# Performance work log

Measured on AMD Instinct MI355X. Metric: run time of the kernel, lower is better.

## Reference

```python
import jax, jax.numpy as jnp
import numpy as np


def setup_inputs() -> dict:
    key = jax.random.key(0)
    k1, k2, k3 = jax.random.split(key, 3)
    B, S, D, H = 16, 2048, 1024, 1024
    inp = jax.random.normal(k1, (B, S, D), dtype=jnp.float32)
    W = jax.random.normal(k2, (3 * H, D), dtype=jnp.float32) * (1.0 / np.sqrt(D))
    b = jax.random.normal(k3, (3 * H,), dtype=jnp.float32) * 0.01
    return {"inp": inp, "W": W, "b": b}


def _forget_mult(z, f):
    # z, f: [B, S, H]; h_t = f_t*z_t + (1-f_t)*h_{t-1}, h_{-1}=0 (hid=None)
    zT = jnp.swapaxes(z, 0, 1)  # [S, B, H]
    fT = jnp.swapaxes(f, 0, 1)

    def step(h, zf):
        z_t, f_t = zf
        h = f_t * z_t + (1.0 - f_t) * h
        return h, h

    h0 = jnp.zeros_like(zT[0])
    _, cT = jax.lax.scan(step, h0, (zT, fT))
    return jnp.swapaxes(cT, 0, 1)  # [B, S, H]


def reference(inp, W, b):
    # window=1, batch_first=True, output_gate=True, backward=False, hid=None
    y = jnp.einsum('bsd,hd->bsh', inp, W) + b  # [B, S, 3H]
    z_gate, f_gate, o_gate = jnp.split(y, 3, axis=2)
    z_gate = jnp.tanh(z_gate)
    f_gate = jax.nn.sigmoid(f_gate)
    c_gate = _forget_mult(z_gate, f_gate)
    output = jax.nn.sigmoid(o_gate) * c_gate
    return output, c_gate[:, -1]
```

## Files before the change

kernel.cpp:

```cpp
#include <hip/hip_runtime.h>


typedef unsigned short ushort_t;
typedef _Float16 half_t;
typedef __bf16 bf16x8 __attribute__((ext_vector_type(8)));
typedef float f32x4 __attribute__((ext_vector_type(4)));
typedef ushort_t us8 __attribute__((ext_vector_type(8)));
typedef half_t f16x4 __attribute__((ext_vector_type(4)));

__device__ __forceinline__ ushort_t f2bf(float f) {
  unsigned int x = __builtin_bit_cast(unsigned int, f);
  x += 0x7fffu + ((x >> 16) & 1u);
  return (ushort_t)(x >> 16);
}
__device__ __forceinline__ float bf2f(ushort_t u) {
  unsigned int x = ((unsigned int)u) << 16;
  return __builtin_bit_cast(float, x);
}
__device__ __forceinline__ void storeg(float* p, float v) { *p = v; }
__device__ __forceinline__ void storeg(half_t* p, float v) { *p = (half_t)v; }

__device__ __forceinline__ f32x4 loadg4(const float* p) {
  return *(const f32x4*)p;
}
__device__ __forceinline__ f32x4 loadg4(const half_t* p) {
  const f16x4 v = *(const f16x4*)p;
  f32x4 r;
  r[0] = (float)v[0]; r[1] = (float)v[1]; r[2] = (float)v[2]; r[3] = (float)v[3];
  return r;
}
__device__ __forceinline__ f32x4 fma4(f32x4 a, f32x4 b, f32x4 c) {
  f32x4 r;
#pragma unroll
  for (int k = 0; k < 4; ++k) r[k] = fmaf(a[k], b[k], c[k]);
  return r;
}

__device__ __forceinline__ float sig_f(float x) { return 1.0f / (1.0f + __expf(-x)); }
__device__ __forceinline__ float tanh_f(float x) { return 1.0f - 2.0f / (1.0f + __expf(2.0f * x)); }

__device__ __forceinline__ void gload_lds16(const ushort_t* g, ushort_t* l) {
  __builtin_amdgcn_global_load_lds(
      (const __attribute__((address_space(1))) void*)g,
      (__attribute__((address_space(3))) void*)l, 16, 0, 0);
}

__global__ void __launch_bounds__(256) cvt_f32_bf16(
    const float* __restrict__ in, ushort_t* __restrict__ out, long n8) {
  long i = (long)blockIdx.x * 256 + threadIdx.x;
  const long stride = (long)gridDim.x * 256;
  for (; i < n8; i += stride) {
    const float4 a = ((const float4*)in)[2 * i];
    const float4 c = ((const float4*)in)[2 * i + 1];
    us8 w;
    w[0] = f2bf(a.x); w[1] = f2bf(a.y); w[2] = f2bf(a.z); w[3] = f2bf(a.w);
    w[4] = f2bf(c.x); w[5] = f2bf(c.y); w[6] = f2bf(c.z); w[7] = f2bf(c.w);
    ((us8*)out)[i] = w;
  }
}

template <typename GT>
__global__ void __launch_bounds__(256) gemm_gates(
    const ushort_t* __restrict__ A, const ushort_t* __restrict__ Wt,
    const float* __restrict__ bias, GT* __restrict__ out,
    int M, int N, int K) {
  constexpr int BK = 64;
  __shared__ __align__(16) ushort_t As[128 * BK];
  __shared__ __align__(16) ushort_t Bs[128 * BK];
  const int tid = threadIdx.x;
  const int lane = tid & 63;
  const int wv = tid >> 6;

  const int bid = blockIdx.x;
  const int nblk = N >> 7;
  const int bn = bid % nblk;
  const int bm = bid / nblk;
  const int m0 = bm << 7, n0 = bn << 7;
  const int wm = (wv >> 1) << 6, wn = (wv & 1) << 6;

  f32x4 acc[4][4] = {};

  const int srow = lane >> 3;
  const int sg = (lane & 7) ^ srow;

  for (int kt = 0; kt < K; kt += BK) {
    __syncthreads();
#pragma unroll
    for (int i = 0; i < 4; ++i) {
      const int rbase = wv * 32 + i * 8;
      gload_lds16(&A[(size_t)(m0 + rbase + srow) * K + kt + sg * 8],
                  &As[rbase * 64]);
      gload_lds16(&Wt[(size_t)(n0 + rbase + srow) * K + kt + sg * 8],
                  &Bs[rbase * 64]);
    }
    __syncthreads();
#pragma unroll
    for (int ks = 0; ks < 2; ++ks) {
      bf16x8 af[4], bfr[4];
#pragma unroll
      for (int t = 0; t < 4; ++t) {
        const int ar = wm + t * 16 + (lane & 15);
        const int ag = ((ks << 2) + (lane >> 4)) ^ (ar & 7);
        af[t] = *(const bf16x8*)&As[ar * 64 + ag * 8];
        const int br = wn + t * 16 + (lane & 15);
        const int bg = ((ks << 2) + (lane >> 4)) ^ (br & 7);
        bfr[t] = *(const bf16x8*)&Bs[br * 64 + bg * 8];
      }
#pragma unroll
      for (int i = 0; i < 4; ++i)
#pragma unroll
        for (int j = 0; j < 4; ++j)
          acc[i][j] =
              __builtin_amdgcn_mfma_f32_16x16x32_bf16(af[i], bfr[j], acc[i][j], 0, 0, 0);
    }
  }

  const int gcat = n0 >> 10;
  const int cn = lane & 15;
  const int cm = (lane >> 4) << 2;
#pragma unroll
  for (int j = 0; j < 4; ++j) {
    const int n = n0 + wn + j * 16 + cn;
    const float bv = bias[n];
#pragma unroll
    for (int i = 0; i < 4; ++i) {
#pragma unroll
      for (int r = 0; r < 4; ++r) {
        const int m = m0 + wm + i * 16 + cm + r;
        const float y = acc[i][j][r] + bv;
        const float v = (gcat == 0) ? tanh_f(y) : sig_f(y);
        storeg(&out[(size_t)m * N + n], v);
      }
    }
  }
}

template <typename GT>
__global__ void __launch_bounds__(256) qrnn_chunk_agg(
    const GT* __restrict__ gates, float* __restrict__ aggG,
    float* __restrict__ aggA, int b0, int S, int H, int C, int L) {
  const int nhb = H >> 10;
  const int hb = blockIdx.x % nhb;
  const int c = (blockIdx.x / nhb) % C;
  const int bl = blockIdx.x / (nhb * C);
  const int h = (hb << 10) + threadIdx.x * 4;
  const int N3 = 3 * H;
  const GT* pz = gates + ((size_t)(bl * S + c * L)) * N3 + h;
  const GT* pf = pz + H;
  f32x4 G = {1.0f, 1.0f, 1.0f, 1.0f};
  f32x4 Aa = {0.0f, 0.0f, 0.0f, 0.0f};
#pragma unroll 4
  for (int j = 0; j < L; ++j) {
    const f32x4 z = loadg4(pz);
    const f32x4 f = loadg4(pf);
    const f32x4 g = 1.0f - f;
    Aa = fma4(g, Aa, f * z);
    G *= g;
    pz += N3;
    pf += N3;
  }
  const size_t idx = ((size_t)((b0 + bl) * C + c)) * H + h;
  *(f32x4*)&aggG[idx] = G;
  *(f32x4*)&aggA[idx] = Aa;
}

template <typename GT>
__global__ void __launch_bounds__(256) qrnn_scan_apply(
    const GT* __restrict__ gates, const float* __restrict__ aggG,
    const float* __restrict__ aggA, float* __restrict__ out,
    int b0, int B, int S, int H, int C, int L) {
  const int nhb = H >> 10;
  const int hb = blockIdx.x % nhb;
  const int c = (blockIdx.x / nhb) % C;
  const int bl = blockIdx.x / (nhb * C);
  const int bg = b0 + bl;
  const int h = (hb << 10) + threadIdx.x * 4;
  const int N3 = 3 * H;

  f32x4 hc = {0.0f, 0.0f, 0.0f, 0.0f};
  for (int cc = 0; cc < c; ++cc) {
    const size_t idx = ((size_t)(bg * C + cc)) * H + h;
    hc = fma4(*(const f32x4*)&aggG[idx], hc, *(const f32x4*)&aggA[idx]);
  }

  const GT* pz = gates + ((size_t)(bl * S + c * L)) * N3 + h;
  const GT* pf = pz + H;
  const GT* po = pf + H;
  size_t oidx = ((size_t)(bg * S + c * L)) * H + h;
#pragma unroll 4
  for (int j = 0; j < L; ++j) {
    const f32x4 z = loadg4(pz);
    const f32x4 f = loadg4(pf);
    const f32x4 o = loadg4(po);
    hc = fma4(1.0f - f, hc, f * z);
    *(f32x4*)&out[oidx] = o * hc;
    pz += N3; pf += N3; po += N3; oidx += H;
  }
  if (c == C - 1) {
    *(f32x4*)&out[(size_t)B * S * H + (size_t)bg * H + h] = hc;
  }
}

template <typename GT>
static void run_groups(const float* inp, const ushort_t* Wbf, const float* b,
                       float* out, ushort_t* Abf, void* gates_ws, float* aggG,
                       float* aggA, int Bg, int B, int S, int H, int K, int C,
                       int L, hipStream_t stream) {
  const int N = 3 * H;
  GT* gates = (GT*)gates_ws;
  for (int b0 = 0; b0 < B; b0 += Bg) {
    const int Mg = Bg * S;
    const long n8 = (long)Mg * K / 8;
    const long cg = (n8 + 255) / 256;
    const int cgrid = (int)(cg < 2048 ? cg : 2048);
    cvt_f32_bf16<<<cgrid, 256, 0, stream>>>(inp + (size_t)b0 * S * K, Abf, n8);
    const int gemm_grid = (Mg / 128) * (N / 128);
    const int scan_grid = Bg * C * (H / 1024);
    gemm_gates<GT><<<gemm_grid, 256, 0, stream>>>(Abf, Wbf, b, gates, Mg, N, K);
    qrnn_chunk_agg<GT><<<scan_grid, 256, 0, stream>>>(
        gates, aggG, aggA, b0, S, H, C, L);
    qrnn_scan_apply<GT><<<scan_grid, 256, 0, stream>>>(
        gates, aggG, aggA, out, b0, B, S, H, C, L);
  }
}

extern "C" void kernel_launch(void* const* d_in, const int* in_sizes, int n_in,
                              void* d_out, int out_size, void* d_ws, size_t ws_size,
                              hipStream_t stream) {
  (void)in_sizes; (void)n_in; (void)out_size;
  const float* inp = (const float*)d_in[0];
  const float* W = (const float*)d_in[1];
  const float* b = (const float*)d_in[2];
  float* out = (float*)d_out;

  constexpr int B = 16, S = 2048, H = 1024, K = 1024;
  constexpr int C = 64, L = S / C;
  const int N3 = 3 * H;

  const size_t agg_elems = (size_t)B * C * H;
  float* aggG = (float*)d_ws;
  float* aggA = aggG + agg_elems;
  ushort_t* Wbf = (ushort_t*)(aggA + agg_elems);
  ushort_t* Abf = Wbf + (size_t)N3 * K;
  const size_t hdr =
      2 * agg_elems * sizeof(float) + (size_t)N3 * K * sizeof(ushort_t);

  int Bg = 0;
  for (int g = 16; g >= 1; g >>= 1) {
    const size_t need = hdr + (size_t)g * S * K * sizeof(ushort_t) +
                        (size_t)g * S * N3 * sizeof(half_t);
    if (need <= ws_size) { Bg = g; break; }
  }
  if (!Bg) return;
  void* gates_ws = (void*)(Abf + (size_t)Bg * S * K);

  {
    const long n8w = (long)N3 * K / 8;
    const long cg = (n8w + 255) / 256;
    const int grid = (int)(cg < 2048 ? cg : 2048);
    cvt_f32_bf16<<<grid, 256, 0, stream>>>(W, Wbf, n8w);
  }

  run_groups<half_t>(inp, Wbf, b, out, Abf, gates_ws, aggG, aggA, Bg,
                     B, S, H, K, C, L, stream);
}
```

Measured before the change: 585.6 us.

## Use 256x256 double-buffered GEMM tile with interleaved LDS staging and MFMA quads

Rewrites the gate GEMM to use 256x256 output tiles on 512 threads (8 waves, each computing a 128x64 sub-tile). A and B tiles are double-buffered in LDS, and the loads for the next k-step are interleaved between four MFMA quadrants with explicit vmcnt waits, barriers and raised wave priority. The goal is to hide global-to-LDS latency and raise data reuse per tile. In exchange it needs 128KB of LDS, which limits the CU to one block, and uses many more accumulator registers.

```diff
diff --git a/kernel.cpp b/kernel.cpp
--- a/kernel.cpp
+++ b/kernel.cpp
@@ -7,6 +7,14 @@
 typedef float f32x4 __attribute__((ext_vector_type(4)));
 typedef ushort_t us8 __attribute__((ext_vector_type(8)));
 typedef half_t f16x4 __attribute__((ext_vector_type(4)));
+
+#define BAR()                                   \
+  do {                                          \
+    asm volatile("" ::: "memory");              \
+    __builtin_amdgcn_s_barrier();               \
+    asm volatile("" ::: "memory");              \
+  } while (0)
+#define WAIT_VMCNT(N) asm volatile("s_waitcnt vmcnt(" #N ")" ::: "memory")
 
 __device__ __forceinline__ ushort_t f2bf(float f) {
   unsigned int x = __builtin_bit_cast(unsigned int, f);
@@ -60,59 +68,117 @@
 }
 
 template <typename GT>
-__global__ void __launch_bounds__(256) gemm_gates(
+__global__ void __launch_bounds__(512, 2) gemm_gates(
     const ushort_t* __restrict__ A, const ushort_t* __restrict__ Wt,
     const float* __restrict__ bias, GT* __restrict__ out,
     int M, int N, int K) {
   constexpr int BK = 64;
-  __shared__ __align__(16) ushort_t As[128 * BK];
-  __shared__ __align__(16) ushort_t Bs[128 * BK];
+  constexpr int TILE = 256 * BK;
+  __shared__ __align__(16) ushort_t As[2 * TILE];
+  __shared__ __align__(16) ushort_t Bs[2 * TILE];
   const int tid = threadIdx.x;
   const int lane = tid & 63;
   const int wv = tid >> 6;
-
-  const int bid = blockIdx.x;
-  const int nblk = N >> 7;
-  const int bn = bid % nblk;
-  const int bm = bid / nblk;
-  const int m0 = bm << 7, n0 = bn << 7;
-  const int wm = (wv >> 1) << 6, wn = (wv & 1) << 6;
-
-  f32x4 acc[4][4] = {};
+  const int nblk = N >> 8;
+  const int bm = blockIdx.x / nblk, bn = blockIdx.x % nblk;
+  const int m0 = bm << 8, n0 = bn << 8;
+  const int wm = (wv >> 2) << 7;
+  const int wn = (wv & 3) << 6;
+  const int NT = K >> 6;
 
   const int srow = lane >> 3;
   const int sg = (lane & 7) ^ srow;
-
-  for (int kt = 0; kt < K; kt += BK) {
-    __syncthreads();
-#pragma unroll
-    for (int i = 0; i < 4; ++i) {
-      const int rbase = wv * 32 + i * 8;
-      gload_lds16(&A[(size_t)(m0 + rbase + srow) * K + kt + sg * 8],
-                  &As[rbase * 64]);
-      gload_lds16(&Wt[(size_t)(n0 + rbase + srow) * K + kt + sg * 8],
-                  &Bs[rbase * 64]);
-    }
-    __syncthreads();
-#pragma unroll
-    for (int ks = 0; ks < 2; ++ks) {
-      bf16x8 af[4], bfr[4];
-#pragma unroll
-      for (int t = 0; t < 4; ++t) {
-        const int ar = wm + t * 16 + (lane & 15);
-        const int ag = ((ks << 2) + (lane >> 4)) ^ (ar & 7);
-        af[t] = *(const bf16x8*)&As[ar * 64 + ag * 8];
-        const int br = wn + t * 16 + (lane & 15);
-        const int bg = ((ks << 2) + (lane >> 4)) ^ (br & 7);
-        bfr[t] = *(const bf16x8*)&Bs[br * 64 + bg * 8];
-      }
-#pragma unroll
-      for (int i = 0; i < 4; ++i)
-#pragma unroll
-        for (int j = 0; j < 4; ++j)
-          acc[i][j] =
-              __builtin_amdgcn_mfma_f32_16x16x32_bf16(af[i], bfr[j], acc[i][j], 0, 0, 0);
-    }
+  const ushort_t* Ag = A + (size_t)m0 * K;
+  const ushort_t* Wg = Wt + (size_t)n0 * K;
+
+  const int fr = lane & 15;
+  const int sl0 = ((lane >> 4) + 0) ^ (lane & 7);
+  const int sl1 = ((lane >> 4) + 4) ^ (lane & 7);
+
+  f32x4 acc[8][4] = {};
+  bf16x8 af[4][2], b0r[2][2], b1r[2][2];
+
+  auto stage_half = [&](const ushort_t* gbase, int row0, ushort_t* lds, int kt) {
+#pragma unroll
+    for (int rnd = 0; rnd < 2; ++rnd) {
+      const int rb = row0 + rnd * 64 + wv * 8;
+      gload_lds16(&gbase[(size_t)(rb + srow) * K + kt + sg * 8], &lds[rb * 64]);
+    }
+  };
+  auto loadA = [&](const ushort_t* Ab, int mi) {
+#pragma unroll
+    for (int mf = 0; mf < 4; ++mf) {
+      const int row = wm + (mi * 4 + mf) * 16 + fr;
+      af[mf][0] = *(const bf16x8*)&Ab[row * 64 + sl0 * 8];
+      af[mf][1] = *(const bf16x8*)&Ab[row * 64 + sl1 * 8];
+    }
+  };
+  auto loadB = [&](bf16x8 (&br)[2][2], const ushort_t* Bb, int ni) {
+#pragma unroll
+    for (int nf = 0; nf < 2; ++nf) {
+      const int row = wn + (ni * 2 + nf) * 16 + fr;
+      br[nf][0] = *(const bf16x8*)&Bb[row * 64 + sl0 * 8];
+      br[nf][1] = *(const bf16x8*)&Bb[row * 64 + sl1 * 8];
+    }
+  };
+  auto quad = [&](bf16x8 (&br)[2][2], int mi, int ni) {
+    __builtin_amdgcn_s_setprio(1);
+#pragma unroll
+    for (int mf = 0; mf < 4; ++mf)
+#pragma unroll
+      for (int nf = 0; nf < 2; ++nf)
+#pragma unroll
+        for (int ks = 0; ks < 2; ++ks)
+          acc[mi * 4 + mf][ni * 2 + nf] = __builtin_amdgcn_mfma_f32_16x16x32_bf16(
+              af[mf][ks], br[nf][ks], acc[mi * 4 + mf][ni * 2 + nf], 0, 0, 0);
+    __builtin_amdgcn_s_setprio(0);
+  };
+
+  stage_half(Ag, 0, As, 0);
+  stage_half(Ag, 128, As, 0);
+  stage_half(Wg, 0, Bs, 0);
+  stage_half(Wg, 128, Bs, 0);
+  if (NT > 1) {
+    stage_half(Wg, 0, Bs + TILE, BK);
+    stage_half(Wg, 128, Bs + TILE, BK);
+    WAIT_VMCNT(4);
+  } else {
+    WAIT_VMCNT(0);
+  }
+  BAR();
+
+  for (int t = 0; t < NT; ++t) {
+    ushort_t* Ab = As + (t & 1) * TILE;
+    ushort_t* Bb = Bs + (t & 1) * TILE;
+    ushort_t* An = As + ((t & 1) ^ 1) * TILE;
+    const int kt1 = (t + 1) * BK, kt2 = (t + 2) * BK;
+    const bool s1 = (t + 1 < NT), s2 = (t + 2 < NT);
+
+    loadA(Ab, 0);
+    loadB(b0r, Bb, 0);
+    if (s1) stage_half(Ag, 0, An, kt1);
+    BAR();
+    quad(b0r, 0, 0);
+    BAR();
+    loadB(b1r, Bb, 1);
+    if (s1) stage_half(Ag, 128, An, kt1);
+    BAR();
+    quad(b1r, 0, 1);
+    BAR();
+    loadA(Ab, 1);
+    if (s2) stage_half(Wg, 0, Bb, kt2);
+    BAR();
+    quad(b1r, 1, 1);
+    BAR();
+    if (s2) stage_half(Wg, 128, Bb, kt2);
+    BAR();
+    quad(b0r, 1, 0);
+    if (s2) {
+      WAIT_VMCNT(4);
+    } else {
+      WAIT_VMCNT(0);
+    }
+    BAR();
   }
 
   const int gcat = n0 >> 10;
@@ -123,7 +189,7 @@
     const int n = n0 + wn + j * 16 + cn;
     const float bv = bias[n];
 #pragma unroll
-    for (int i = 0; i < 4; ++i) {
+    for (int i = 0; i < 8; ++i) {
 #pragma unroll
       for (int r = 0; r < 4; ++r) {
         const int m = m0 + wm + i * 16 + cm + r;
@@ -214,9 +280,9 @@
     const long cg = (n8 + 255) / 256;
     const int cgrid = (int)(cg < 2048 ? cg : 2048);
     cvt_f32_bf16<<<cgrid, 256, 0, stream>>>(inp + (size_t)b0 * S * K, Abf, n8);
-    const int gemm_grid = (Mg / 128) * (N / 128);
+    const int gemm_grid = (Mg / 256) * (N / 256);
     const int scan_grid = Bg * C * (H / 1024);
-    gemm_gates<GT><<<gemm_grid, 256, 0, stream>>>(Abf, Wbf, b, gates, Mg, N, K);
+    gemm_gates<GT><<<gemm_grid, 512, 0, stream>>>(Abf, Wbf, b, gates, Mg, N, K);
     qrnn_chunk_agg<GT><<<scan_grid, 256, 0, stream>>>(
         gates, aggG, aggA, b0, S, H, C, L);
     qrnn_scan_apply<GT><<<scan_grid, 256, 0, stream>>>(
```

New measurement: 608.3 us. +3.9%, slower.

## Add separate chunk-prefix scan kernel, double chunk count, use nontemporal output stores

Applied to the files above, without the earlier changes.

Adds a small qrnn_prefix kernel that computes each chunk's starting hidden state once and writes it to a new aggH buffer. Before this, every apply block re-walked all earlier chunk aggregates, which is quadratic in the chunk count. With that cost gone, the chunk count rises from 64 to 128, giving the apply and aggregate kernels more parallelism. Output stores become nontemporal to reduce cache pollution. The cost is an extra kernel launch, a serial prefix kernel with few blocks, and more workspace.

```diff
diff --git a/kernel.cpp b/kernel.cpp
--- a/kernel.cpp
+++ b/kernel.cpp
@@ -34,6 +34,9 @@
 #pragma unroll
   for (int k = 0; k < 4; ++k) r[k] = fmaf(a[k], b[k], c[k]);
   return r;
+}
+__device__ __forceinline__ void store4_nt(float* p, f32x4 v) {
+  __builtin_nontemporal_store(v, (f32x4*)p);
 }
 
 __device__ __forceinline__ float sig_f(float x) { return 1.0f / (1.0f + __expf(-x)); }
@@ -164,11 +167,26 @@
   *(f32x4*)&aggA[idx] = Aa;
 }
 
+__global__ void __launch_bounds__(256) qrnn_prefix(
+    const float* __restrict__ aggG, const float* __restrict__ aggA,
+    float* __restrict__ aggH, int b0, int H, int C) {
+  const int nhb = H >> 10;
+  const int b = b0 + blockIdx.x / nhb;
+  const int hb = blockIdx.x % nhb;
+  const int h = (hb << 10) + threadIdx.x * 4;
+  f32x4 hc = {0.0f, 0.0f, 0.0f, 0.0f};
+#pragma unroll 4
+  for (int c = 0; c < C; ++c) {
+    const size_t idx = ((size_t)(b * C + c)) * H + h;
+    *(f32x4*)&aggH[idx] = hc;
+    hc = fma4(*(const f32x4*)&aggG[idx], hc, *(const f32x4*)&aggA[idx]);
+  }
+}
+
 template <typename GT>
 __global__ void __launch_bounds__(256) qrnn_scan_apply(
-    const GT* __restrict__ gates, const float* __restrict__ aggG,
-    const float* __restrict__ aggA, float* __restrict__ out,
-    int b0, int B, int S, int H, int C, int L) {
+    const GT* __restrict__ gates, const float* __restrict__ aggH,
+    float* __restrict__ out, int b0, int B, int S, int H, int C, int L) {
   const int nhb = H >> 10;
   const int hb = blockIdx.x % nhb;
   const int c = (blockIdx.x / nhb) % C;
@@ -177,11 +195,7 @@
   const int h = (hb << 10) + threadIdx.x * 4;
   const int N3 = 3 * H;
 
-  f32x4 hc = {0.0f, 0.0f, 0.0f, 0.0f};
-  for (int cc = 0; cc < c; ++cc) {
-    const size_t idx = ((size_t)(bg * C + cc)) * H + h;
-    hc = fma4(*(const f32x4*)&aggG[idx], hc, *(const f32x4*)&aggA[idx]);
-  }
+  f32x4 hc = *(const f32x4*)&aggH[((size_t)(bg * C + c)) * H + h];
 
   const GT* pz = gates + ((size_t)(bl * S + c * L)) * N3 + h;
   const GT* pf = pz + H;
@@ -193,7 +207,7 @@
     const f32x4 f = loadg4(pf);
     const f32x4 o = loadg4(po);
     hc = fma4(1.0f - f, hc, f * z);
-    *(f32x4*)&out[oidx] = o * hc;
+    store4_nt(&out[oidx], o * hc);
     pz += N3; pf += N3; po += N3; oidx += H;
   }
   if (c == C - 1) {
@@ -204,8 +218,8 @@
 template <typename GT>
 static void run_groups(const float* inp, const ushort_t* Wbf, const float* b,
                        float* out, ushort_t* Abf, void* gates_ws, float* aggG,
-                       float* aggA, int Bg, int B, int S, int H, int K, int C,
-                       int L, hipStream_t stream) {
+                       float* aggA, float* aggH, int Bg, int B, int S, int H,
+                       int K, int C, int L, hipStream_t stream) {
   const int N = 3 * H;
   GT* gates = (GT*)gates_ws;
   for (int b0 = 0; b0 < B; b0 += Bg) {
@@ -219,8 +233,9 @@
     gemm_gates<GT><<<gemm_grid, 256, 0, stream>>>(Abf, Wbf, b, gates, Mg, N, K);
     qrnn_chunk_agg<GT><<<scan_grid, 256, 0, stream>>>(
         gates, aggG, aggA, b0, S, H, C, L);
+    qrnn_prefix<<<Bg * (H / 1024), 256, 0, stream>>>(aggG, aggA, aggH, b0, H, C);
     qrnn_scan_apply<GT><<<scan_grid, 256, 0, stream>>>(
-        gates, aggG, aggA, out, b0, B, S, H, C, L);
+        gates, aggH, out, b0, B, S, H, C, L);
   }
 }
 
@@ -234,16 +249,17 @@
   float* out = (float*)d_out;
 
   constexpr int B = 16, S = 2048, H = 1024, K = 1024;
-  constexpr int C = 64, L = S / C;
+  constexpr int C = 128, L = S / C;
   const int N3 = 3 * H;
 
   const size_t agg_elems = (size_t)B * C * H;
   float* aggG = (float*)d_ws;
   float* aggA = aggG + agg_elems;
-  ushort_t* Wbf = (ushort_t*)(aggA + agg_elems);
+  float* aggH = aggA + agg_elems;
+  ushort_t* Wbf = (ushort_t*)(aggH + agg_elems);
   ushort_t* Abf = Wbf + (size_t)N3 * K;
   const size_t hdr =
-      2 * agg_elems * sizeof(float) + (size_t)N3 * K * sizeof(ushort_t);
+      3 * agg_elems * sizeof(float) + (size_t)N3 * K * sizeof(ushort_t);
 
   int Bg = 0;
   for (int g = 16; g >= 1; g >>= 1) {
@@ -261,6 +277,6 @@
     cvt_f32_bf16<<<grid, 256, 0, stream>>>(W, Wbf, n8w);
   }
 
-  run_groups<half_t>(inp, Wbf, b, out, Abf, gates_ws, aggG, aggA, Bg,
+  run_groups<half_t>(inp, Wbf, b, out, Abf, gates_ws, aggG, aggA, aggH, Bg,
                      B, S, H, K, C, L, stream);
 }
```

Measured after the change: 590.4 us. No clear change (+0.8%).
